# Performance work log

Hardware: AMD Instinct MI355X
Metric: run time of the kernel (lower is better)

Reference implementation:

```python
import jax, jax.numpy as jnp
import numpy as np


def setup_inputs() -> dict:
    key = jax.random.key(0)
    ks = jax.random.split(key, 5)
    B, C_in, C_out, H, W, k = 16, 64, 64, 256, 256, 16
    scale = 1.0 / (C_in * C_out)
    return {
        "u": jax.random.normal(ks[0], (B, C_in, H, W), dtype=jnp.float32),
        "W_pos_re": scale * jax.random.normal(ks[1], (C_in, C_out, k, k), dtype=jnp.float32),
        "W_pos_im": scale * jax.random.normal(ks[2], (C_in, C_out, k, k), dtype=jnp.float32),
        "W_neg_re": scale * jax.random.normal(ks[3], (C_in, C_out, k, k), dtype=jnp.float32),
        "W_neg_im": scale * jax.random.normal(ks[4], (C_in, C_out, k, k), dtype=jnp.float32),
    }


def reference(u, W_pos_re, W_pos_im, W_neg_re, W_neg_im):
    B, C_in, H, W = u.shape
    C_out = W_pos_re.shape[1]
    k = W_pos_re.shape[2]
    W_half = W // 2 + 1
    k_h = min(k, H // 2)
    k_w = min(k, W_half)

    R_pos = (W_pos_re + 1j * W_pos_im)[:, :, :k_h, :k_w]  # (C_in, C_out, k_h, k_w)
    R_neg = (W_neg_re + 1j * W_neg_im)[:, :, :k_h, :k_w]

    u_hat = jnp.fft.rfft2(u, norm="ortho")  # (B, C_in, H, W_half) complex

    # spectral multiply on retained modes only
    top = jnp.einsum("bchw,cohw->bohw", u_hat[:, :, :k_h, :k_w], R_pos)
    bot = jnp.einsum("bchw,cohw->bohw", u_hat[:, :, H - k_h:, :k_w], R_neg)

    v_hat = jnp.zeros((B, C_out, H, W_half), dtype=u_hat.dtype)
    v_hat = v_hat.at[:, :, :k_h, :k_w].set(top)
    v_hat = v_hat.at[:, :, H - k_h:, :k_w].set(bot)

    return jnp.fft.irfft2(v_hat, s=(H, W), norm="ortho")  # (B, C_out, H, W) real
```

## Files before the change

### kernel.cpp

```cpp
#include <hip/hip_runtime.h>


#define B_    16
#define H_    256
#define W_    256

#define OFF_CT 0
#define OFF_ST 256
#define OFF_RP 512
#define RP_SZ  (4096*512*2)
#define OFF_U  (OFF_RP + RP_SZ)
#define U_SZ   (512*1024*2)
#define OFF_V  (OFF_U + U_SZ)

#define UTP   260
#define TWOPI_256 0.024543692606170259f

typedef const __attribute__((address_space(1))) void g_void;
typedef __attribute__((address_space(3))) void l_void;

__device__ __forceinline__ void load_lds16(const float* g, float* l) {
    __builtin_amdgcn_global_load_lds((g_void*)g, (l_void*)l, 16, 0, 0);
}

__global__ __launch_bounds__(256) void k_repack(const float* __restrict__ wpr,
                                                const float* __restrict__ wpi,
                                                const float* __restrict__ wnr,
                                                const float* __restrict__ wni,
                                                float* __restrict__ ws) {
    int co = blockIdx.x, t = threadIdx.x;
    if (co == 0) {
        double a = 2.0 * 3.14159265358979323846 * (double)t / 256.0;
        ws[OFF_CT + t] = (float)cos(a);
        ws[OFF_ST + t] = (float)sin(a);
    }
    int wm = t & 15;
    float norm = (wm == 0 ? 1.f : 2.f) * (1.f / 65536.f);
    size_t src = (size_t)co * 256 + t;
    float2* rp = (float2*)(ws + OFF_RP) + (size_t)co * 512;
    rp[t]       = make_float2(wpr[src] * norm, wpi[src] * norm);
    rp[t + 256] = make_float2(wnr[src] * norm, wni[src] * norm);
}

__global__ __launch_bounds__(256) void k_fwd1(const float* __restrict__ u,
                                              float* __restrict__ P) {
    __shared__ __align__(16) float ut[32][UTP];
    int t = threadIdx.x;
    int bc = blockIdx.x >> 3, ch = blockIdx.x & 7;
    const float* ub = u + (size_t)bc * 65536 + ch * 8192;
    int lane = t & 63, w = t >> 6;
    #pragma unroll
    for (int k = 0; k < 8; ++k)
        load_lds16(ub + (w * 8 + k) * 256 + lane * 4, &ut[w * 8 + k][0]);

    int h = lane & 7, r8 = lane >> 3;
    int rowc = w * 8 + r8;
    int wm0 = 2 * h, wm1 = wm0 + 1;
    float s0v, c0v, s1v, c1v;
    __sincosf(TWOPI_256 * (float)wm0, &s0v, &c0v);
    __sincosf(TWOPI_256 * (float)wm1, &s1v, &c1v);
    float r0r = c0v, r0i = -s0v;
    float r1r = c1v, r1i = -s1v;
    float bs  = (h & 1) ? -1.f : 1.f;
    float dsg = (h & 1) ? 1.f : -1.f;

    float p0r = 0.f, p0i = 0.f, p1r = 0.f, p1i = 0.f;
    float t0r = 1.f, t0i = 0.f, t1r = 1.f, t1i = 0.f;

    asm volatile("s_waitcnt vmcnt(0)" ::: "memory");

    const float* rowp = &ut[rowc][0];
    #pragma unroll 4
    for (int bat = 0; bat < 16; ++bat) {
        const float* rp = rowp + 4 * bat;
        float4 q0 = *(const float4*)(rp);
        float4 q1 = *(const float4*)(rp + 64);
        float4 q2 = *(const float4*)(rp + 128);
        float4 q3 = *(const float4*)(rp + 192);
        #define PROC_(u0, u1, u2, u3) {                                   \
            float a_ = (u0) + (u2), b_ = (u1) + (u3);                     \
            float c_ = (u0) - (u2), d_ = (u1) - (u3);                     \
            float g0 = fmaf(bs, b_, a_);                                  \
            float g1r = c_, g1i = dsg * d_;                               \
            p0r = fmaf(g0, t0r, p0r);                                     \
            p0i = fmaf(g0, t0i, p0i);                                     \
            p1r = fmaf(g1r, t1r, fmaf(-g1i, t1i, p1r));                   \
            p1i = fmaf(g1r, t1i, fmaf( g1i, t1r, p1i));                   \
            float n0r = t0r * r0r - t0i * r0i;                            \
            float n0i = t0r * r0i + t0i * r0r;                            \
            float n1r = t1r * r1r - t1i * r1i;                            \
            float n1i = t1r * r1i + t1i * r1r;                            \
            t0r = n0r; t0i = n0i; t1r = n1r; t1i = n1i; }
        PROC_(q0.x, q1.x, q2.x, q3.x)
        PROC_(q0.y, q1.y, q2.y, q3.y)
        PROC_(q0.z, q1.z, q2.z, q3.z)
        PROC_(q0.w, q1.w, q2.w, q3.w)
        #undef PROC_
    }
    int y = ch * 32 + rowc;
    ((float4*)P)[((size_t)bc * 256 + y) * 8 + h] = make_float4(p0r, p0i, p1r, p1i);
}

__global__ __launch_bounds__(256) void k_fwd2(const float* __restrict__ P,
                                              float* __restrict__ ws) {
    __shared__ float Pl[256][36];
    int t = threadIdx.x, bc = blockIdx.x;
    const float4* Pg = (const float4*)(P + (size_t)bc * 8192);
    #pragma unroll
    for (int k = 0; k < 8; ++k) {
        int f4 = t + 256 * k;
        int y = f4 >> 3, q = f4 & 7;
        *(float4*)&Pl[y][q * 4] = Pg[f4];
    }
    __syncthreads();

    int wm = t & 15;
    int v  = t >> 4;
    int m1 = ((v & 3) << 2) | (v >> 2);
    float sv, cv;
    __sincosf(TWOPI_256 * (float)m1, &sv, &cv);
    float r1r = cv, r1i = -sv;
    __sincosf(TWOPI_256 * (float)(m1 - 16), &sv, &cv);
    float r2r = cv, r2i = -sv;
    float t1r = 1.f, t1i = 0.f, t2r = 1.f, t2i = 0.f;
    float U1r = 0.f, U1i = 0.f, U2r = 0.f, U2i = 0.f;
    int md = m1 & 3;
    #pragma unroll 4
    for (int yy = 0; yy < 64; ++yy) {
        float2 P0 = *(float2*)&Pl[yy][2 * wm];
        float2 P1 = *(float2*)&Pl[yy + 64][2 * wm];
        float2 P2 = *(float2*)&Pl[yy + 128][2 * wm];
        float2 P3 = *(float2*)&Pl[yy + 192][2 * wm];
        float ar = P0.x + P2.x, ai = P0.y + P2.y;
        float br = P1.x + P3.x, bi = P1.y + P3.y;
        float cr = P0.x - P2.x, ci = P0.y - P2.y;
        float dr = P1.x - P3.x, di = P1.y - P3.y;
        float gr, gi;
        if (md == 0)      { gr = ar + br; gi = ai + bi; }
        else if (md == 1) { gr = cr + di; gi = ci - dr; }
        else if (md == 2) { gr = ar - br; gi = ai - bi; }
        else              { gr = cr - di; gi = ci + dr; }
        U1r = fmaf(gr, t1r, fmaf(-gi, t1i, U1r));
        U1i = fmaf(gr, t1i, fmaf( gi, t1r, U1i));
        U2r = fmaf(gr, t2r, fmaf(-gi, t2i, U2r));
        U2i = fmaf(gr, t2i, fmaf( gi, t2r, U2i));
        float n1r = t1r * r1r - t1i * r1i, n1i = t1r * r1i + t1i * r1r;
        float n2r = t2r * r2r - t2i * r2i, n2i = t2r * r2i + t2i * r2r;
        t1r = n1r; t1i = n1i; t2r = n2r; t2i = n2i;
    }
    float2* U = (float2*)(ws + OFF_U);
    U[(size_t)(m1 * 16 + wm) * 1024 + bc]        = make_float2(U1r, U1i);
    U[(size_t)((m1 + 16) * 16 + wm) * 1024 + bc] = make_float2(U2r, U2i);
}

__global__ __launch_bounds__(256) void k_cgemm(float* __restrict__ ws) {
    __shared__ float2 Ul[1024];
    int mw = blockIdx.x, t = threadIdx.x;
    const float2* Ug = (const float2*)(ws + OFF_U) + (size_t)mw * 1024;
    #pragma unroll
    for (int k = 0; k < 4; ++k) Ul[t + 256 * k] = Ug[t + 256 * k];
    __syncthreads();
    int o = t & 63, bq = t >> 6;
    const float2* rp = (const float2*)(ws + OFF_RP);
    float ar[4] = {0.f, 0.f, 0.f, 0.f}, ai[4] = {0.f, 0.f, 0.f, 0.f};
    #pragma unroll 4
    for (int c = 0; c < 64; ++c) {
        float2 R = rp[(size_t)(c * 64 + o) * 512 + mw];
        #pragma unroll
        for (int j = 0; j < 4; ++j) {
            float2 Uv = Ul[(bq * 4 + j) * 64 + c];
            ar[j] = fmaf(Uv.x, R.x, fmaf(-Uv.y, R.y, ar[j]));
            ai[j] = fmaf(Uv.x, R.y, fmaf( Uv.y, R.x, ai[j]));
        }
    }
    float2* Vg = (float2*)(ws + OFF_V);
    #pragma unroll
    for (int j = 0; j < 4; ++j)
        Vg[(size_t)((bq * 4 + j) * 64 + o) * 512 + mw] = make_float2(ar[j], ai[j]);
}

__global__ __launch_bounds__(256) void k_inv(const float* __restrict__ ws,
                                             float* __restrict__ out) {
    __shared__ float Vl[16][68];
    __shared__ float Tl[4][16][36];
    __shared__ float ct[256], st[256];
    int t = threadIdx.x;
    int bo = blockIdx.x >> 2, q = blockIdx.x & 3;
    ct[t] = ws[OFF_CT + t];
    st[t] = ws[OFF_ST + t];
    {
        const float2* Vg = (const float2*)(ws + OFF_V) + (size_t)bo * 512;
        float2 v0 = Vg[t];
        float2 v1 = Vg[t + 256];
        int m = t >> 4, wmv = t & 15;
        Vl[wmv][2 * m]        = v0.x;  Vl[wmv][2 * m + 1]        = v0.y;
        Vl[wmv][2 * (m + 16)] = v1.x;  Vl[wmv][2 * (m + 16) + 1] = v1.y;
    }
    __syncthreads();

    int wm4 = t & 15, yb = t >> 4;
    int y0 = q * 16 + yb;
    float vr[32], vi[32];
    #pragma unroll
    for (int m = 0; m < 32; ++m) { vr[m] = Vl[wm4][2 * m]; vi[m] = Vl[wm4][2 * m + 1]; }
    float cy = ct[y0], sy = st[y0];
    float T0r=0,T0i=0,T1r=0,T1i=0,T2r=0,T2i=0,T3r=0,T3i=0;
    float tr = 1.f, ti = 0.f;
    #pragma unroll
    for (int m = 0; m < 32; ++m) {
        if (m == 16) {
            int i16 = (4096 - 16 * y0) & 255;
            tr = ct[i16]; ti = st[i16];
        }
        float hr = vr[m] * tr - vi[m] * ti;
        float hi = vr[m] * ti + vi[m] * tr;
        const int md = m & 3;
        T0r += hr; T0i += hi;
        if (md == 0)      { T1r += hr; T1i += hi; T2r += hr; T2i += hi; T3r += hr; T3i += hi; }
        else if (md == 1) { T1r -= hi; T1i += hr; T2r -= hr; T2i -= hi; T3r += hi; T3i -= hr; }
        else if (md == 2) { T1r -= hr; T1i -= hi; T2r += hr; T2i += hi; T3r -= hr; T3i -= hi; }
        else              { T1r += hi; T1i -= hr; T2r -= hr; T2i -= hi; T3r -= hi; T3i += hr; }
        float nr = tr * cy - ti * sy, ni = tr * sy + ti * cy;
        tr = nr; ti = ni;
    }
    Tl[0][yb][wm4] = T0r; Tl[0][yb][16 + wm4] = T0i;
    Tl[1][yb][wm4] = T1r; Tl[1][yb][16 + wm4] = T1i;
    Tl[2][yb][wm4] = T2r; Tl[2][yb][16 + wm4] = T2i;
    Tl[3][yb][wm4] = T3r; Tl[3][yb][16 + wm4] = T3i;
    __syncthreads();

    int l = t & 63, wv = t >> 6;
    float c0[16], s0[16];
    #pragma unroll
    for (int wm = 0; wm < 16; ++wm) {
        int idx = (wm * l) & 255;
        c0[wm] = ct[idx]; s0[wm] = st[idx];
    }
    float* ob = out + (size_t)bo * 65536;
    for (int yi = 0; yi < 16; ++yi) {
        int y = wv * 64 + q * 16 + yi;
        float TR[16], TI[16];
        const float4* rowv = (const float4*)&Tl[wv][yi][0];
        #pragma unroll
        for (int qq = 0; qq < 4; ++qq) {
            float4 a = rowv[qq];
            TR[4*qq]=a.x; TR[4*qq+1]=a.y; TR[4*qq+2]=a.z; TR[4*qq+3]=a.w;
            float4 b = rowv[qq + 4];
            TI[4*qq]=b.x; TI[4*qq+1]=b.y; TI[4*qq+2]=b.z; TI[4*qq+3]=b.w;
        }
        #pragma unroll
        for (int k = 0; k < 4; ++k) {
            float a = 0.f;
            #pragma unroll
            for (int wm = 0; wm < 16; ++wm) {
                int p = (k * wm) & 3;
                if (p == 0)      a +=  TR[wm] * c0[wm] - TI[wm] * s0[wm];
                else if (p == 1) a += -TR[wm] * s0[wm] - TI[wm] * c0[wm];
                else if (p == 2) a += -TR[wm] * c0[wm] + TI[wm] * s0[wm];
                else             a +=  TR[wm] * s0[wm] + TI[wm] * c0[wm];
            }
            ob[(size_t)y * 256 + 64 * k + l] = a;
        }
    }
}

extern "C" void kernel_launch(void* const* d_in, const int* in_sizes, int n_in,
                              void* d_out, int out_size, void* d_ws, size_t ws_size,
                              hipStream_t stream) {
    const float* u   = (const float*)d_in[0];
    const float* wpr = (const float*)d_in[1];
    const float* wpi = (const float*)d_in[2];
    const float* wnr = (const float*)d_in[3];
    const float* wni = (const float*)d_in[4];
    float* out = (float*)d_out;
    float* ws  = (float*)d_ws;
    float* P   = (float*)d_out;

    hipLaunchKernelGGL(k_repack,  dim3(4096), dim3(256), 0, stream, wpr, wpi, wnr, wni, ws);
    hipLaunchKernelGGL(k_fwd1,    dim3(8192), dim3(256), 0, stream, u, P);
    hipLaunchKernelGGL(k_fwd2,    dim3(1024), dim3(256), 0, stream, P, ws);
    hipLaunchKernelGGL(k_cgemm,   dim3(512),  dim3(256), 0, stream, ws);
    hipLaunchKernelGGL(k_inv,     dim3(4096), dim3(256), 0, stream, ws, out);
}
```

Measured before the change: 233.6 us.

## Fold weight repack into forward kernel and transpose spectral workspace layouts

Removes the separate repack launch by adding 512 extra blocks to k_fwd1 that repack the weights, laid out per mode (mode-major, then c_in x c_out). The U and V intermediates are transposed so that k_fwd2 writes U contiguously per (b,c) and k_cgemm reads weights and writes V contiguously per mode. The strided access moves to the k_cgemm U gather and the k_inv V gather, and the repack blocks now read the source weights with a 256-float stride.

```diff
diff --git a/kernel.cpp b/kernel.cpp
--- a/kernel.cpp
+++ b/kernel.cpp
@@ -8,9 +8,9 @@
 #define OFF_CT 0
 #define OFF_ST 256
 #define OFF_RP 512
-#define RP_SZ  (4096*512*2)
+#define RP_SZ  (512*4096*2)
 #define OFF_U  (OFF_RP + RP_SZ)
-#define U_SZ   (512*1024*2)
+#define U_SZ   (1024*512*2)
 #define OFF_V  (OFF_U + U_SZ)
 
 #define UTP   260
@@ -23,29 +23,39 @@
     __builtin_amdgcn_global_load_lds((g_void*)g, (l_void*)l, 16, 0, 0);
 }
 
-__global__ __launch_bounds__(256) void k_repack(const float* __restrict__ wpr,
-                                                const float* __restrict__ wpi,
-                                                const float* __restrict__ wnr,
-                                                const float* __restrict__ wni,
-                                                float* __restrict__ ws) {
-    int co = blockIdx.x, t = threadIdx.x;
-    if (co == 0) {
-        double a = 2.0 * 3.14159265358979323846 * (double)t / 256.0;
-        ws[OFF_CT + t] = (float)cos(a);
-        ws[OFF_ST + t] = (float)sin(a);
-    }
-    int wm = t & 15;
-    float norm = (wm == 0 ? 1.f : 2.f) * (1.f / 65536.f);
-    size_t src = (size_t)co * 256 + t;
-    float2* rp = (float2*)(ws + OFF_RP) + (size_t)co * 512;
-    rp[t]       = make_float2(wpr[src] * norm, wpi[src] * norm);
-    rp[t + 256] = make_float2(wnr[src] * norm, wni[src] * norm);
-}
-
 __global__ __launch_bounds__(256) void k_fwd1(const float* __restrict__ u,
+                                              const float* __restrict__ wpr,
+                                              const float* __restrict__ wpi,
+                                              const float* __restrict__ wnr,
+                                              const float* __restrict__ wni,
+                                              float* __restrict__ ws,
                                               float* __restrict__ P) {
     __shared__ __align__(16) float ut[32][UTP];
     int t = threadIdx.x;
+
+    if (blockIdx.x >= 8192) {
+        int mw = blockIdx.x - 8192;
+        int m = mw >> 4, wmc = mw & 15;
+        const float* wr; const float* wi; int i;
+        if (m < 16) { wr = wpr; wi = wpi; i = m; }
+        else        { wr = wnr; wi = wni; i = m - 16; }
+        if (mw == 0) {
+            double a = 2.0 * 3.14159265358979323846 * (double)t / 256.0;
+            ws[OFF_CT + t] = (float)cos(a);
+            ws[OFF_ST + t] = (float)sin(a);
+        }
+        float norm = (wmc == 0 ? 1.f : 2.f) * (1.f / 65536.f);
+        int off = i * 16 + wmc;
+        float2* rp = (float2*)(ws + OFF_RP) + (size_t)mw * 4096;
+        #pragma unroll
+        for (int k = 0; k < 16; ++k) {
+            int co = t + 256 * k;
+            rp[co] = make_float2(wr[(size_t)co * 256 + off] * norm,
+                                 wi[(size_t)co * 256 + off] * norm);
+        }
+        return;
+    }
+
     int bc = blockIdx.x >> 3, ch = blockIdx.x & 7;
     const float* ub = u + (size_t)bc * 65536 + ch * 8192;
     int lane = t & 63, w = t >> 6;
@@ -148,24 +158,27 @@
         float n2r = t2r * r2r - t2i * r2i, n2i = t2r * r2i + t2i * r2r;
         t1r = n1r; t1i = n1i; t2r = n2r; t2i = n2i;
     }
-    float2* U = (float2*)(ws + OFF_U);
-    U[(size_t)(m1 * 16 + wm) * 1024 + bc]        = make_float2(U1r, U1i);
-    U[(size_t)((m1 + 16) * 16 + wm) * 1024 + bc] = make_float2(U2r, U2i);
+    float2* U = (float2*)(ws + OFF_U) + (size_t)bc * 512;
+    U[m1 * 16 + wm]          = make_float2(U1r, U1i);
+    U[(m1 + 16) * 16 + wm]   = make_float2(U2r, U2i);
 }
 
 __global__ __launch_bounds__(256) void k_cgemm(float* __restrict__ ws) {
     __shared__ float2 Ul[1024];
     int mw = blockIdx.x, t = threadIdx.x;
-    const float2* Ug = (const float2*)(ws + OFF_U) + (size_t)mw * 1024;
-    #pragma unroll
-    for (int k = 0; k < 4; ++k) Ul[t + 256 * k] = Ug[t + 256 * k];
+    const float2* Ug = (const float2*)(ws + OFF_U);
+    #pragma unroll
+    for (int k = 0; k < 4; ++k) {
+        int bcv = t + 256 * k;
+        Ul[bcv] = Ug[(size_t)bcv * 512 + mw];
+    }
     __syncthreads();
     int o = t & 63, bq = t >> 6;
-    const float2* rp = (const float2*)(ws + OFF_RP);
+    const float2* rp = (const float2*)(ws + OFF_RP) + (size_t)mw * 4096;
     float ar[4] = {0.f, 0.f, 0.f, 0.f}, ai[4] = {0.f, 0.f, 0.f, 0.f};
     #pragma unroll 4
     for (int c = 0; c < 64; ++c) {
-        float2 R = rp[(size_t)(c * 64 + o) * 512 + mw];
+        float2 R = rp[c * 64 + o];
         #pragma unroll
         for (int j = 0; j < 4; ++j) {
             float2 Uv = Ul[(bq * 4 + j) * 64 + c];
@@ -173,10 +186,10 @@
             ai[j] = fmaf(Uv.x, R.y, fmaf( Uv.y, R.x, ai[j]));
         }
     }
-    float2* Vg = (float2*)(ws + OFF_V);
+    float2* Vg = (float2*)(ws + OFF_V) + (size_t)mw * 1024;
     #pragma unroll
     for (int j = 0; j < 4; ++j)
-        Vg[(size_t)((bq * 4 + j) * 64 + o) * 512 + mw] = make_float2(ar[j], ai[j]);
+        Vg[(bq * 4 + j) * 64 + o] = make_float2(ar[j], ai[j]);
 }
 
 __global__ __launch_bounds__(256) void k_inv(const float* __restrict__ ws,
@@ -189,9 +202,9 @@
     ct[t] = ws[OFF_CT + t];
     st[t] = ws[OFF_ST + t];
     {
-        const float2* Vg = (const float2*)(ws + OFF_V) + (size_t)bo * 512;
-        float2 v0 = Vg[t];
-        float2 v1 = Vg[t + 256];
+        const float2* Vg = (const float2*)(ws + OFF_V);
+        float2 v0 = Vg[(size_t)t * 1024 + bo];
+        float2 v1 = Vg[(size_t)(t + 256) * 1024 + bo];
         int m = t >> 4, wmv = t & 15;
         Vl[wmv][2 * m]        = v0.x;  Vl[wmv][2 * m + 1]        = v0.y;
         Vl[wmv][2 * (m + 16)] = v1.x;  Vl[wmv][2 * (m + 16) + 1] = v1.y;
@@ -276,9 +289,8 @@
     float* ws  = (float*)d_ws;
     float* P   = (float*)d_out;
 
-    hipLaunchKernelGGL(k_repack,  dim3(4096), dim3(256), 0, stream, wpr, wpi, wnr, wni, ws);
-    hipLaunchKernelGGL(k_fwd1,    dim3(8192), dim3(256), 0, stream, u, P);
-    hipLaunchKernelGGL(k_fwd2,    dim3(1024), dim3(256), 0, stream, P, ws);
-    hipLaunchKernelGGL(k_cgemm,   dim3(512),  dim3(256), 0, stream, ws);
-    hipLaunchKernelGGL(k_inv,     dim3(4096), dim3(256), 0, stream, ws, out);
-}
+    hipLaunchKernelGGL(k_fwd1,  dim3(8704), dim3(256), 0, stream, u, wpr, wpi, wnr, wni, ws, P);
+    hipLaunchKernelGGL(k_fwd2,  dim3(1024), dim3(256), 0, stream, P, ws);
+    hipLaunchKernelGGL(k_cgemm, dim3(512),  dim3(256), 0, stream, ws);
+    hipLaunchKernelGGL(k_inv,   dim3(4096), dim3(256), 0, stream, ws, out);
+}
```

After: 221.6 us. 1.05x faster.
